# Optimization experiments

Hardware: AMD Instinct MI355X
Metric: run time of the kernel (lower is better)

The kernel has to match this reference:

```python
import jax, jax.numpy as jnp
import numpy as np

N, E, IN_DIM, HID, HEADS, LAYERS, NUM_STORES = 50000, 800000, 64, 128, 16, 3, 50
DH = HID // HEADS  # per-head dim = 8
EPS = 1e-5


def setup_inputs() -> dict:
    key = jax.random.key(0)
    ks = iter(jax.random.split(key, 40))
    def nrm(shape, scale):
        return jax.random.normal(next(ks), shape, dtype=jnp.float32) * scale
    inp = {}
    inp['x'] = jax.random.normal(next(ks), (N, IN_DIM), dtype=jnp.float32)
    inp['edge_index'] = jax.random.randint(next(ks), (2, E), 0, N, dtype=jnp.int32)
    inp['edge_weight'] = jax.random.uniform(next(ks), (E, 1), dtype=jnp.float32)
    inp['store_mask'] = jax.random.randint(next(ks), (N,), 0, NUM_STORES, dtype=jnp.int32)
    # input_proj: Linear + GELU + LayerNorm
    inp['in_W'] = nrm((IN_DIM, HID), IN_DIM ** -0.5)
    inp['in_b'] = jnp.zeros((HID,), jnp.float32)
    inp['in_g'] = jnp.ones((HID,), jnp.float32)
    inp['in_beta'] = jnp.zeros((HID,), jnp.float32)
    # 3 stacked GATv2 layers (stacked leading dim = layer)
    s = HID ** -0.5
    inp['gat_Wl'] = nrm((LAYERS, HID, HID), s)
    inp['gat_bl'] = jnp.zeros((LAYERS, HID), jnp.float32)
    inp['gat_Wr'] = nrm((LAYERS, HID, HID), s)
    inp['gat_br'] = jnp.zeros((LAYERS, HID), jnp.float32)
    inp['gat_We'] = nrm((LAYERS, 1, HID), 1.0)
    inp['gat_att'] = nrm((LAYERS, HEADS, DH), DH ** -0.5)
    inp['gat_bias'] = jnp.zeros((LAYERS, HID), jnp.float32)
    inp['blk_g'] = jnp.ones((LAYERS, HID), jnp.float32)
    inp['blk_b'] = jnp.zeros((LAYERS, HID), jnp.float32)
    # per-store context gate + final norm
    inp['ctx_W'] = nrm((HID, HID), s)
    inp['ctx_b'] = jnp.zeros((HID,), jnp.float32)
    inp['fin_g'] = jnp.ones((HID,), jnp.float32)
    inp['fin_b'] = jnp.zeros((HID,), jnp.float32)
    return inp


def layernorm(x, g, b):
    mu = jnp.mean(x, axis=-1, keepdims=True)
    v = jnp.mean((x - mu) ** 2, axis=-1, keepdims=True)
    return (x - mu) * jax.lax.rsqrt(v + EPS) * g + b


def gatv2_layer(x, src, dst, ea, Wl, bl, Wr, br, We, att, bias):
    # x: [N, HID]; src/dst: [Et]; ea: [Et, 1]
    n = x.shape[0]
    xl = (x @ Wl + bl).reshape(n, HEADS, DH)   # source transform
    xr = (x @ Wr + br).reshape(n, HEADS, DH)   # target transform
    ee = (ea @ We).reshape(-1, HEADS, DH)      # edge-attr embedding
    e = jax.nn.leaky_relu(xl[src] + xr[dst] + ee, 0.2)  # [Et, H, D]
    logit = jnp.einsum('ehd,hd->eh', e, att)             # [Et, H]
    # segment softmax over incoming edges of each target node
    mx = jax.ops.segment_max(logit, dst, num_segments=n)
    p = jnp.exp(logit - mx[dst])
    Z = jax.ops.segment_sum(p, dst, num_segments=n)
    alpha = p / (Z[dst] + 1e-16)
    msg = alpha[:, :, None] * xl[src]                    # [Et, H, D]
    agg = jax.ops.segment_sum(msg, dst, num_segments=n)  # [N, H, D]
    return agg.reshape(n, HEADS * DH) + bias


def forward(x, edge_index, edge_weight, store_mask, in_W, in_b, in_g, in_beta,
            gat_Wl, gat_bl, gat_Wr, gat_br, gat_We, gat_att, gat_bias,
            blk_g, blk_b, ctx_W, ctx_b, fin_g, fin_b):
    n = x.shape[0]
    h = layernorm(jax.nn.gelu(x @ in_W + in_b, approximate=False), in_g, in_beta)
    src, dst = edge_index[0], edge_index[1]
    # PyG add_self_loops with fill_value='mean': per-target mean of incoming edge attrs
    deg = jax.ops.segment_sum(jnp.ones(src.shape, h.dtype), dst, num_segments=n)
    loop_attr = jax.ops.segment_sum(edge_weight, dst, num_segments=n) / jnp.maximum(deg, 1.0)[:, None]
    loops = jnp.arange(n, dtype=src.dtype)
    srcf = jnp.concatenate([src, loops])
    dstf = jnp.concatenate([dst, loops])
    eaf = jnp.concatenate([edge_weight, loop_attr], axis=0)
    for l in range(LAYERS):  # residual block: post-norm residual around conv
        m = gatv2_layer(h, srcf, dstf, eaf, gat_Wl[l], gat_bl[l], gat_Wr[l], gat_br[l],
                        gat_We[l], gat_att[l], gat_bias[l])
        h = layernorm(h + m, blk_g[l], blk_b[l])
    # per-store segmented mean -> sigmoid gate -> scatter back
    cnt = jax.ops.segment_sum(jnp.ones((n,), h.dtype), store_mask, num_segments=NUM_STORES)
    means = jax.ops.segment_sum(h, store_mask, num_segments=NUM_STORES) / jnp.maximum(cnt, 1.0)[:, None]
    gate = jax.nn.sigmoid(means @ ctx_W + ctx_b)
    h = h + (gate * means)[store_mask]
    return layernorm(h, fin_g, fin_b)


def reference(x, edge_index, edge_weight, store_mask, in_W, in_b, in_g, in_beta,
              gat_Wl, gat_bl, gat_Wr, gat_br, gat_We, gat_att, gat_bias,
              blk_g, blk_b, ctx_W, ctx_b, fin_g, fin_b):
    return forward(x, edge_index, edge_weight, store_mask, in_W, in_b, in_g, in_beta,
                   gat_Wl, gat_bl, gat_Wr, gat_br, gat_We, gat_att, gat_bias,
                   blk_g, blk_b, ctx_W, ctx_b, fin_g, fin_b)
```

## Files before the change

### kernel.cpp

```cpp
#include <hip/hip_runtime.h>
#include <math.h>

#define NN 50000
#define EE 800000
#define ET (EE + NN)
#define HID 128
#define NSTORE 50
#define NBL 196
#define CNT_B 3125
#define WCV_B 192
#define IWC_B 32
#define SCT_B2 1661
#define GEMB 391
#define IPB 782
#define SSB 512
#define WB2 6250

typedef unsigned short ushort_t;
typedef unsigned int u32;
typedef __attribute__((ext_vector_type(8))) short bf8;
typedef __attribute__((ext_vector_type(4))) float f4;
typedef __attribute__((ext_vector_type(2))) float f2;
typedef __attribute__((ext_vector_type(4))) unsigned int u4;

__device__ __forceinline__ ushort_t f2b(float f) {
    union { float f; unsigned int i; } v; v.f = f;
    unsigned int r = (v.i + 0x7fffu + ((v.i >> 16) & 1u)) >> 16;
    return (ushort_t)r;
}
__device__ __forceinline__ f2 b2f2v(unsigned int u) {
    union { unsigned int i; float f; } lo, hi;
    lo.i = u << 16; hi.i = u & 0xffff0000u;
    f2 r; r.x = lo.f; r.y = hi.f; return r;
}
__device__ __forceinline__ unsigned int pk2(float lo, float hi) {
    return (unsigned int)f2b(lo) | ((unsigned int)f2b(hi) << 16);
}
__device__ __forceinline__ f2 max2(f2 a, f2 b) {
#if __has_builtin(__builtin_elementwise_max)
    return __builtin_elementwise_max(a, b);
#else
    f2 r; r.x = fmaxf(a.x, b.x); r.y = fmaxf(a.y, b.y); return r;
#endif
}

__global__ __launch_bounds__(256) void k_build(const int* __restrict__ ei, const float* __restrict__ ew,
                                               const float* __restrict__ inW,
                                               const float* __restrict__ gWl, const float* __restrict__ gWr,
                                               ushort_t* __restrict__ inWt,
                                               ushort_t* __restrict__ Wlt, ushort_t* __restrict__ Wrt,
                                               u32* __restrict__ packed, int* __restrict__ rank) {
    int b = blockIdx.x, t = threadIdx.x;
    if (b < CNT_B) {
        int i = b * 256 + t;
        int dst = ei[EE + i];
        unsigned int wfix = __float2uint_rn(ew[i] * 262144.0f);
        unsigned int old = atomicAdd(&packed[dst], (1u << 24) | wfix);
        rank[i] = (int)(old >> 24);
        return;
    }
    if (b < CNT_B + WCV_B) {
        int i = (b - CNT_B) * 256 + t;
        int l = i >> 14, r = i & 16383, nn2 = r >> 7, k = r & 127;
        Wlt[i] = f2b(gWl[(size_t)l * 16384 + k * 128 + nn2]);
        Wrt[i] = f2b(gWr[(size_t)l * 16384 + k * 128 + nn2]);
        return;
    }
    {
        int i = (b - CNT_B - WCV_B) * 256 + t;
        int c = i >> 6, k = i & 63;
        inWt[i] = f2b(inW[k * 128 + c]);
    }
}

__global__ __launch_bounds__(256) void k_psum(const u32* __restrict__ packed, int* __restrict__ bsum) {
    int t = threadIdx.x, bidx = blockIdx.x;
    int i = bidx * 256 + t;
    int v = (i < NN) ? (int)(packed[i] >> 24) + 1 : 0;
#pragma unroll
    for (int d = 1; d < 64; d <<= 1) v += __shfl_xor(v, d);
    __shared__ int ws4[4];
    if ((t & 63) == 0) ws4[t >> 6] = v;
    __syncthreads();
    if (t == 0) bsum[bidx] = ws4[0] + ws4[1] + ws4[2] + ws4[3];
}

__global__ __launch_bounds__(256) void k_offs2(const u32* __restrict__ packed,
                                               const int* __restrict__ bsum, int* __restrict__ offs) {
    __shared__ int bws[4];
    __shared__ int wsum4[4];
    int t = threadIdx.x, bidx = blockIdx.x;
    int i = bidx * 256 + t;
    int v = (i < NN) ? (int)(packed[i] >> 24) + 1 : 0;
    int lane = t & 63, w = t >> 6;

    int bv = (t < bidx) ? bsum[t] : 0;
#pragma unroll
    for (int d = 1; d < 64; d <<= 1) bv += __shfl_xor(bv, d);
    if (lane == 0) bws[w] = bv;

    int sc = v;
#pragma unroll
    for (int d = 1; d < 64; d <<= 1) {
        int u = __shfl_up(sc, d);
        if (lane >= d) sc += u;
    }
    if (lane == 63) wsum4[w] = sc;
    __syncthreads();
    int base = bws[0] + bws[1] + bws[2] + bws[3];
    int wo = 0;
    for (int k = 0; k < w; ++k) wo += wsum4[k];
    if (i < NN) offs[i] = base + wo + sc - v;
    if (bidx == 0 && t == 0) offs[NN] = ET;
}

__global__ __launch_bounds__(512) void k_inproj(const float* __restrict__ X,
                                                const ushort_t* __restrict__ Wt,
                                                const float* __restrict__ bias,
                                                const float* __restrict__ g,
                                                const float* __restrict__ be,
                                                ushort_t* __restrict__ hb) {
    const int K = 64;
    __shared__ float s1[2][64], s2[2][64];
    int t = threadIdx.x;
    int w = t >> 6, lane = t & 63;
    int cw = w & 1, rw = w >> 1;
    int q = lane >> 4, l16 = lane & 15;
    int row0 = blockIdx.x * 64 + rw * 16;
    int col0 = cw * 64;
    bf8 z; for (int k = 0; k < 8; ++k) z[k] = 0;

    bf8 bfr[2][4];
#pragma unroll
    for (int kk = 0; kk < 2; ++kk)
#pragma unroll
        for (int j = 0; j < 4; ++j)
            bfr[kk][j] = *(const bf8*)(Wt + (size_t)(col0 + j * 16 + l16) * K + kk * 32 + q * 8);

    f4 acc[4];
#pragma unroll
    for (int j = 0; j < 4; ++j) acc[j] = (f4)(0.f);

#pragma unroll
    for (int kk = 0; kk < 2; ++kk) {
        bf8 af;
        int r = row0 + l16;
        if (r < NN) {
            const float* xp = X + (size_t)r * K + kk * 32 + q * 8;
            f4 a = *(const f4*)xp;
            f4 c = *(const f4*)(xp + 4);
            u4 up; up.x = pk2(a.x, a.y); up.y = pk2(a.z, a.w);
            up.z = pk2(c.x, c.y); up.w = pk2(c.z, c.w);
            af = *(bf8*)&up;
        } else af = z;
#pragma unroll
        for (int j = 0; j < 4; ++j)
            acc[j] = __builtin_amdgcn_mfma_f32_16x16x32_bf16(af, bfr[kk][j], acc[j], 0, 0, 0);
    }
#pragma unroll
    for (int j = 0; j < 4; ++j) {
        float bv = bias[col0 + j * 16 + l16];
#pragma unroll
        for (int r = 0; r < 4; ++r) {
            float v = acc[j][r] + bv;
            v = 0.5f * v * (1.f + erff(v * 0.70710678118654752f));
            acc[j][r] = v;
        }
    }
#pragma unroll
    for (int r = 0; r < 4; ++r) {
        float sm = acc[0][r] + acc[1][r] + acc[2][r] + acc[3][r];
        float sq = acc[0][r] * acc[0][r] + acc[1][r] * acc[1][r]
                 + acc[2][r] * acc[2][r] + acc[3][r] * acc[3][r];
#pragma unroll
        for (int k = 1; k < 16; k <<= 1) { sm += __shfl_xor(sm, k); sq += __shfl_xor(sq, k); }
        if (l16 == 0) {
            int rl = rw * 16 + q * 4 + r;
            s1[cw][rl] = sm; s2[cw][rl] = sq;
        }
    }
    __syncthreads();
#pragma unroll
    for (int r = 0; r < 4; ++r) {
        int rl = rw * 16 + q * 4 + r;
        int gr = blockIdx.x * 64 + rl;
        if (gr >= NN) continue;
        float sm = s1[0][rl] + s1[1][rl];
        float sq = s2[0][rl] + s2[1][rl];
        float mu = sm * (1.f / 128.f);
        float var = sq * (1.f / 128.f) - mu * mu;
        float rinv = rsqrtf(var + 1e-5f);
#pragma unroll
        for (int j = 0; j < 4; ++j) {
            int gc = col0 + j * 16 + l16;
            float v = (acc[j][r] - mu) * rinv * g[gc] + be[gc];
            hb[(size_t)gr * HID + gc] = f2b(v);
        }
    }
}

__global__ __launch_bounds__(512) void k_gemm2(const ushort_t* __restrict__ A,
                                               const ushort_t* __restrict__ Wt0,
                                               const ushort_t* __restrict__ Wt1,
                                               const float* __restrict__ b0,
                                               const float* __restrict__ b1,
                                               ushort_t* __restrict__ o0,
                                               ushort_t* __restrict__ o1, int n,
                                               const int* __restrict__ ei,
                                               const float* __restrict__ ew,
                                               const int* __restrict__ offs,
                                               const u32* __restrict__ packed,
                                               const int* __restrict__ rank,
                                               int2* __restrict__ csr) {
    int bid = blockIdx.x;
    if (bid >= GEMB) {
        int i = (bid - GEMB) * 512 + threadIdx.x;
        if (i < EE) {
            int src = ei[i], dst = ei[EE + i];
            int pos = offs[dst] + rank[i];
            int2 v; v.x = src << 8; v.y = __float_as_int(ew[i]);
            csr[pos] = v;
        } else if (i < ET) {
            int nd = i - EE;
            u32 p = packed[nd];
            int deg = (int)(p >> 24);
            float wsf = (float)(p & 0xFFFFFFu) * (1.0f / 262144.0f);
            float la = wsf / fmaxf((float)deg, 1.0f);
            int pos = offs[nd + 1] - 1;
            int2 v; v.x = nd << 8; v.y = __float_as_int(la);
            csr[pos] = v;
        }
        return;
    }
    const int K = 128;
    __shared__ char As[128 * 256];
    int t = threadIdx.x;
    int row0 = bid * 128;
    bf8 z; for (int k = 0; k < 8; ++k) z[k] = 0;

    {
        int row = t >> 2, cq = t & 3;
        const ushort_t* srcp = A + (size_t)(row0 + row) * K + cq * 8;
        int swz = (row & 7) << 4;
        char* dst = As + row * 256;
        bool ok = (row0 + row) < n;
#pragma unroll
        for (int k = 0; k < 4; ++k) {
            bf8 v = ok ? *(const bf8*)(srcp + k * 32) : z;
            *(bf8*)(dst + ((k * 64 + cq * 16) ^ swz)) = v;
        }
    }
    __syncthreads();

    int w = t >> 6, lane = t & 63;
    int side = w >> 2, rw = (w >> 1) & 1, cw = w & 1;
    const ushort_t* Wt = side ? Wt1 : Wt0;
    const float* bias = side ? b1 : b0;
    ushort_t* outb = side ? o1 : o0;
    int q = lane >> 4, l16 = lane & 15;
    int col0 = cw * 64;

    f4 acc[4][4];
#pragma unroll
    for (int i = 0; i < 4; ++i)
#pragma unroll
        for (int j = 0; j < 4; ++j) acc[i][j] = (f4)(0.f);

#pragma unroll
    for (int kk = 0; kk < 4; ++kk) {
        bf8 bfk[4];
#pragma unroll
        for (int j = 0; j < 4; ++j)
            bfk[j] = *(const bf8*)(Wt + (size_t)(col0 + j * 16 + l16) * K + kk * 32 + q * 8);
        bf8 af[4];
#pragma unroll
        for (int i = 0; i < 4; ++i) {
            int r = rw * 64 + i * 16 + l16;
            af[i] = *(const bf8*)(As + r * 256 + ((kk * 64 + q * 16) ^ ((r & 7) << 4)));
        }
#pragma unroll
        for (int i = 0; i < 4; ++i)
#pragma unroll
            for (int j = 0; j < 4; ++j)
                acc[i][j] = __builtin_amdgcn_mfma_f32_16x16x32_bf16(af[i], bfk[j], acc[i][j], 0, 0, 0);
    }
#pragma unroll
    for (int i = 0; i < 4; ++i) {
        int gr0 = row0 + rw * 64 + i * 16 + q * 4;
#pragma unroll
        for (int j = 0; j < 4; ++j) {
            int gc = col0 + j * 16 + l16;
            float bv = bias[gc];
#pragma unroll
            for (int r = 0; r < 4; ++r) {
                int gr = gr0 + r;
                if (gr < n) outb[(size_t)gr * HID + gc] = f2b(acc[i][j][r] + bv);
            }
        }
    }
}

__global__ __launch_bounds__(256) void k_attn(const ushort_t* __restrict__ xl,
                                              const ushort_t* __restrict__ xr,
                                              ushort_t* __restrict__ hb,
                                              const int* __restrict__ offs,
                                              const int2* __restrict__ csr,
                                              const float* __restrict__ We,
                                              const float* __restrict__ att,
                                              const float* __restrict__ gbias,
                                              const float* __restrict__ g,
                                              const float* __restrict__ b,
                                              int n0) {
    int wid = n0 + ((blockIdx.x * 256 + threadIdx.x) >> 6);
    int lane = threadIdx.x & 63;
    if (wid >= NN) return;
    int hd = lane & 15;
    int grp = lane >> 4;
    int dbase = hd * 8;
    int db2 = hd * 16;
    size_t base = (size_t)wid * HID;

    f2 xr2[4], at2[4], we2[4];
    {
        u4 uxr = *(const u4*)(xr + base + dbase);
        xr2[0] = b2f2v(uxr.x); xr2[1] = b2f2v(uxr.y);
        xr2[2] = b2f2v(uxr.z); xr2[3] = b2f2v(uxr.w);
        f4 a0 = *(const f4*)(att + dbase), a1 = *(const f4*)(att + dbase + 4);
        at2[0].x = a0.x; at2[0].y = a0.y; at2[1].x = a0.z; at2[1].y = a0.w;
        at2[2].x = a1.x; at2[2].y = a1.y; at2[3].x = a1.z; at2[3].y = a1.w;
        f4 w0 = *(const f4*)(We + dbase), w1 = *(const f4*)(We + dbase + 4);
        we2[0].x = w0.x; we2[0].y = w0.y; we2[1].x = w0.z; we2[1].y = w0.w;
        we2[2].x = w1.x; we2[2].y = w1.y; we2[3].x = w1.z; we2[3].y = w1.w;
    }
    int p0 = offs[wid], p1 = offs[wid + 1];
    float Z = 0.f;
    f2 acc2[4];
#pragma unroll
    for (int q = 0; q < 4; ++q) { acc2[q].x = 0.f; acc2[q].y = 0.f; }

#define LOADQ(UX, EA, VM)                                                      \
    {                                                                          \
        int ei_ = e + grp;                                                     \
        VM = (ei_ < p1);                                                       \
        int2 m2_ = csr[VM ? ei_ : (p1 - 1)];                                   \
        EA = __int_as_float(m2_.y);                                            \
        UX = *(const u4*)((const char*)xl + (unsigned)m2_.x + db2);            \
    }

#define COMPQ(UX, EA, VM)                                                      \
    {                                                                          \
        f2 x2_[4];                                                             \
        x2_[0] = b2f2v(UX.x); x2_[1] = b2f2v(UX.y);                            \
        x2_[2] = b2f2v(UX.z); x2_[3] = b2f2v(UX.w);                            \
        f2 lg2_; lg2_.x = 0.f; lg2_.y = 0.f;                                   \
        _Pragma("unroll")                                                      \
        for (int q_ = 0; q_ < 4; ++q_) {                                       \
            f2 t_ = (x2_[q_] + xr2[q_]) + EA * we2[q_];                        \
            t_ = max2(t_, t_ * 0.2f);                                          \
            lg2_ += at2[q_] * t_;                                              \
        }                                                                      \
        float w_ = VM ? __expf(lg2_.x + lg2_.y) : 0.f;                         \
        Z += w_;                                                               \
        _Pragma("unroll")                                                      \
        for (int q_ = 0; q_ < 4; ++q_) acc2[q_] += w_ * x2_[q_];               \
    }

    {
        u4 uxA, uxB; float eaA, eaB; bool vA, vB;
        int e = p0;
        LOADQ(uxA, eaA, vA)
        e += 4;
        while (e < p1) {
            LOADQ(uxB, eaB, vB)
            e += 4;
            COMPQ(uxA, eaA, vA)
            if (e >= p1) { COMPQ(uxB, eaB, vB) goto redux; }
            LOADQ(uxA, eaA, vA)
            e += 4;
            COMPQ(uxB, eaB, vB)
        }
        COMPQ(uxA, eaA, vA)
    }
redux:;
#undef LOADQ
#undef COMPQ

    Z += __shfl_xor(Z, 16); Z += __shfl_xor(Z, 32);
#pragma unroll
    for (int q = 0; q < 4; ++q) {
        acc2[q].x += __shfl_xor(acc2[q].x, 16);
        acc2[q].x += __shfl_xor(acc2[q].x, 32);
        acc2[q].y += __shfl_xor(acc2[q].y, 16);
        acc2[q].y += __shfl_xor(acc2[q].y, 32);
    }
    float inv = 1.f / (Z + 1e-16f);
    float acc[8] = {acc2[0].x, acc2[0].y, acc2[1].x, acc2[1].y,
                    acc2[2].x, acc2[2].y, acc2[3].x, acc2[3].y};

    u4 uh = *(const u4*)(hb + base + dbase);
    f2 hr0 = b2f2v(uh.x), hr1 = b2f2v(uh.y), hr2 = b2f2v(uh.z), hr3 = b2f2v(uh.w);
    float hres[8] = {hr0.x, hr0.y, hr1.x, hr1.y, hr2.x, hr2.y, hr3.x, hr3.y};
    f4 gb0 = *(const f4*)(gbias + dbase), gb1 = *(const f4*)(gbias + dbase + 4);
    float gb8[8] = {gb0.x, gb0.y, gb0.z, gb0.w, gb1.x, gb1.y, gb1.z, gb1.w};
    float o[8], sm = 0.f, sq = 0.f;
#pragma unroll
    for (int q = 0; q < 8; ++q) {
        o[q] = acc[q] * inv + gb8[q] + hres[q];
        sm += o[q]; sq += o[q] * o[q];
    }
#pragma unroll
    for (int k = 1; k < 16; k <<= 1) { sm += __shfl_xor(sm, k); sq += __shfl_xor(sq, k); }
    float mu = sm * (1.f / 128.f);
    float var = sq * (1.f / 128.f) - mu * mu;
    float rinv = rsqrtf(var + 1e-5f);
    f4 g0 = *(const f4*)(g + dbase), g1 = *(const f4*)(g + dbase + 4);
    float g8[8] = {g0.x, g0.y, g0.z, g0.w, g1.x, g1.y, g1.z, g1.w};
    f4 b0 = *(const f4*)(b + dbase), b1 = *(const f4*)(b + dbase + 4);
    float b8[8] = {b0.x, b0.y, b0.z, b0.w, b1.x, b1.y, b1.z, b1.w};
    float v8[8];
#pragma unroll
    for (int q = 0; q < 8; ++q) v8[q] = (o[q] - mu) * rinv * g8[q] + b8[q];
    if (grp == 0) {
        u4 hu;
        hu.x = pk2(v8[0], v8[1]); hu.y = pk2(v8[2], v8[3]);
        hu.z = pk2(v8[4], v8[5]); hu.w = pk2(v8[6], v8[7]);
        *(u4*)(hb + base + dbase) = hu;
    }
}

__global__ __launch_bounds__(256) void k_store_sum(const ushort_t* __restrict__ hb,
                                                   const int* __restrict__ mask,
                                                   float* __restrict__ psums,
                                                   int* __restrict__ pcnts) {
    __shared__ float ls[NSTORE * HID];
    __shared__ int lc[NSTORE];
    int t = threadIdx.x, bidx = blockIdx.x;
    for (int i = t; i < NSTORE * HID; i += 256) ls[i] = 0.f;
    if (t < NSTORE) lc[t] = 0;
    __syncthreads();
    int wid = bidx * 4 + (t >> 6);
    int lane = t & 63;
    int nw = SSB * 4;
    int d0 = lane * 2;
    for (int node = wid; node < NN; node += nw) {
        int s = mask[node];
        unsigned int hv = ((const unsigned int*)(hb + (size_t)node * HID))[lane];
        f2 v = b2f2v(hv);
        atomicAdd(&ls[s * HID + d0], v.x);
        atomicAdd(&ls[s * HID + d0 + 1], v.y);
        if (lane == 0) atomicAdd(&lc[s], 1);
    }
    __syncthreads();
    for (int i = t; i < NSTORE * HID; i += 256) psums[(size_t)bidx * (NSTORE * HID) + i] = ls[i];
    if (t < NSTORE) pcnts[bidx * NSTORE + t] = lc[t];
}

__global__ __launch_bounds__(256) void k_gate(const float* __restrict__ psums,
                                              const int* __restrict__ pcnts,
                                              const float* __restrict__ ctxW,
                                              const float* __restrict__ ctxb,
                                              float* __restrict__ gm) {
    __shared__ float h1[HID];
    __shared__ float mloc[HID];
    __shared__ int cw4[4];
    int s = blockIdx.x, t = threadIdx.x;
    int d = t & 127, half = t >> 7;
    float s0 = 0.f, s1 = 0.f, s2 = 0.f, s3 = 0.f;
    for (int b = half * 4; b < SSB; b += 8) {
        s0 += psums[(size_t)(b + 0) * (NSTORE * HID) + s * HID + d];
        s1 += psums[(size_t)(b + 1) * (NSTORE * HID) + s * HID + d];
        s2 += psums[(size_t)(b + 2) * (NSTORE * HID) + s * HID + d];
        s3 += psums[(size_t)(b + 3) * (NSTORE * HID) + s * HID + d];
    }
    float sum = (s0 + s1) + (s2 + s3);
    int c = pcnts[t * NSTORE + s] + pcnts[(t + 256) * NSTORE + s];
#pragma unroll
    for (int k = 1; k < 64; k <<= 1) c += __shfl_xor(c, k);
    if ((t & 63) == 0) cw4[t >> 6] = c;
    if (half) h1[d] = sum;
    __syncthreads();
    if (half == 0) {
        float tot = sum + h1[d];
        float cnt = fmaxf((float)(cw4[0] + cw4[1] + cw4[2] + cw4[3]), 1.f);
        mloc[d] = tot / cnt;
    }
    __syncthreads();
    if (half == 0) {
        float acc = ctxb[d];
        for (int j = 0; j < HID; ++j) acc += mloc[j] * ctxW[j * HID + d];
        float gate = 1.f / (1.f + __expf(-acc));
        gm[s * HID + d] = gate * mloc[d];
    }
}

__global__ __launch_bounds__(256) void k_final(const ushort_t* __restrict__ hb,
                                               const int* __restrict__ mask,
                                               const float* __restrict__ gm,
                                               const float* __restrict__ g,
                                               const float* __restrict__ b,
                                               float* __restrict__ out) {
    int wid = (blockIdx.x * 256 + threadIdx.x) >> 6;
    int lane = threadIdx.x & 63;
    if (wid >= NN) return;
    size_t base = (size_t)wid * HID;
    int s = mask[wid];
    int d0 = lane * 2, d1 = d0 + 1;
    unsigned int hv = ((const unsigned int*)(hb + base))[lane];
    f2 hvv = b2f2v(hv);
    float v0 = hvv.x + gm[s * HID + d0];
    float v1 = hvv.y + gm[s * HID + d1];
    float sm = v0 + v1, sq = v0 * v0 + v1 * v1;
#pragma unroll
    for (int k = 1; k < 64; k <<= 1) { sm += __shfl_xor(sm, k); sq += __shfl_xor(sq, k); }
    float mu = sm * (1.f / 128.f);
    float var = sq * (1.f / 128.f) - mu * mu;
    float r = rsqrtf(var + 1e-5f);
    out[base + d0] = (v0 - mu) * r * g[d0] + b[d0];
    out[base + d1] = (v1 - mu) * r * g[d1] + b[d1];
}

extern "C" void kernel_launch(void* const* d_in, const int* in_sizes, int n_in,
                              void* d_out, int out_size, void* d_ws, size_t ws_size,
                              hipStream_t stream) {
    const float* x      = (const float*)d_in[0];
    const int*   ei     = (const int*)d_in[1];
    const float* ew     = (const float*)d_in[2];
    const int*   smask  = (const int*)d_in[3];
    const float* inW    = (const float*)d_in[4];
    const float* inb    = (const float*)d_in[5];
    const float* ing    = (const float*)d_in[6];
    const float* inbeta = (const float*)d_in[7];
    const float* gWl    = (const float*)d_in[8];
    const float* gbl    = (const float*)d_in[9];
    const float* gWr    = (const float*)d_in[10];
    const float* gbr    = (const float*)d_in[11];
    const float* gWe    = (const float*)d_in[12];
    const float* gatt   = (const float*)d_in[13];
    const float* gbias  = (const float*)d_in[14];
    const float* blkg   = (const float*)d_in[15];
    const float* blkb   = (const float*)d_in[16];
    const float* ctxW   = (const float*)d_in[17];
    const float* ctxb   = (const float*)d_in[18];
    const float* fing   = (const float*)d_in[19];
    const float* finb   = (const float*)d_in[20];
    float* out = (float*)d_out;

    float* ws = (float*)d_ws;
    size_t o = 0;
    int2*     csr    = (int2*)(ws + o);     o += (size_t)ET * 2;
    float*    gm     = ws + o;              o += NSTORE * HID;
    int*      offs   = (int*)(ws + o);      o += 50004;
    int*      rank   = (int*)(ws + o);      o += EE;
    ushort_t* hb     = (ushort_t*)(ws + o); o += (size_t)NN * HID / 2;
    ushort_t* xlb    = (ushort_t*)(ws + o); o += (size_t)NN * HID / 2;
    ushort_t* xrb    = (ushort_t*)(ws + o); o += (size_t)NN * HID / 2;
    ushort_t* inWt   = (ushort_t*)(ws + o); o += 128 * 64 / 2;
    ushort_t* Wlt    = (ushort_t*)(ws + o); o += 3 * 128 * 128 / 2;
    ushort_t* Wrt    = (ushort_t*)(ws + o); o += 3 * 128 * 128 / 2;
    int*      bsum   = (int*)(ws + o);      o += 256;
    float*    psums  = ws + o;              o += (size_t)SSB * NSTORE * HID;
    int*      pcnts  = (int*)(ws + o);      o += SSB * NSTORE;
    u32*      packed = (u32*)(ws + o);      o += NN;
    size_t zbytes = (size_t)NN * 4;

    hipMemsetAsync((void*)packed, 0, zbytes, stream);

    const int WB = NN / 4;

    k_build<<<CNT_B + WCV_B + IWC_B, 256, 0, stream>>>(ei, ew, inW, gWl, gWr,
                                                       inWt, Wlt, Wrt, packed, rank);
    k_psum<<<NBL, 256, 0, stream>>>(packed, bsum);
    k_offs2<<<NBL, 256, 0, stream>>>(packed, bsum, offs);
    k_inproj<<<IPB, 512, 0, stream>>>(x, inWt, inb, ing, inbeta, hb);

    for (int l = 0; l < 3; ++l) {
        int nb = GEMB + (l == 0 ? SCT_B2 : 0);
        k_gemm2<<<nb, 512, 0, stream>>>(hb, Wlt + (size_t)l * HID * HID, Wrt + (size_t)l * HID * HID,
                                        gbl + l * HID, gbr + l * HID, xlb, xrb, NN,
                                        ei, ew, offs, packed, rank, csr);
        k_attn<<<WB2, 256, 0, stream>>>(xlb, xrb, hb, offs, csr,
                                        gWe + l * HID, gatt + l * HID, gbias + l * HID,
                                        blkg + l * HID, blkb + l * HID, 0);
        k_attn<<<WB2, 256, 0, stream>>>(xlb, xrb, hb, offs, csr,
                                        gWe + l * HID, gatt + l * HID, gbias + l * HID,
                                        blkg + l * HID, blkb + l * HID, 25000);
    }

    k_store_sum<<<SSB, 256, 0, stream>>>(hb, smask, psums, pcnts);
    k_gate<<<NSTORE, 256, 0, stream>>>(psums, pcnts, ctxW, ctxb, gm);
    k_final<<<WB, 256, 0, stream>>>(hb, smask, gm, fing, finb, out);
}
```

Measured before the change: 476.9 us.

## Retile GEMM to 64-row blocks, merge attention launches, widen gate kernel

The dual-projection GEMM now uses 64-row tiles, with each wave computing 16 rows across all 128 columns instead of a 64x64 sub-tile. This doubles the block count for better occupancy and load balance. The two half-range attention launches per layer become a single launch. The store-gate reduction uses 1024 threads per block to shorten its serial psum loop, and the final LayerNorm writes float2 vectors. The trade-off is that each wave now reloads its weight fragments from global memory, and the smaller tiles reuse the A tile less.

```diff
diff --git a/kernel.cpp b/kernel.cpp
--- a/kernel.cpp
+++ b/kernel.cpp
@@ -11,10 +11,9 @@
 #define WCV_B 192
 #define IWC_B 32
 #define SCT_B2 1661
-#define GEMB 391
+#define GEMB2 782
 #define IPB 782
 #define SSB 512
-#define WB2 6250
 
 typedef unsigned short ushort_t;
 typedef unsigned int u32;
@@ -213,8 +212,8 @@
                                                const int* __restrict__ rank,
                                                int2* __restrict__ csr) {
     int bid = blockIdx.x;
-    if (bid >= GEMB) {
-        int i = (bid - GEMB) * 512 + threadIdx.x;
+    if (bid >= GEMB2) {
+        int i = (bid - GEMB2) * 512 + threadIdx.x;
         if (i < EE) {
             int src = ei[i], dst = ei[EE + i];
             int pos = offs[dst] + rank[i];
@@ -233,69 +232,58 @@
         return;
     }
     const int K = 128;
-    __shared__ char As[128 * 256];
+    __shared__ char As[64 * 256];
     int t = threadIdx.x;
-    int row0 = bid * 128;
+    int row0 = bid * 64;
     bf8 z; for (int k = 0; k < 8; ++k) z[k] = 0;
 
     {
-        int row = t >> 2, cq = t & 3;
-        const ushort_t* srcp = A + (size_t)(row0 + row) * K + cq * 8;
+        int row = t >> 3, cq = t & 7;
+        const ushort_t* srcp = A + (size_t)(row0 + row) * K + cq * 16;
         int swz = (row & 7) << 4;
         char* dst = As + row * 256;
         bool ok = (row0 + row) < n;
 #pragma unroll
-        for (int k = 0; k < 4; ++k) {
-            bf8 v = ok ? *(const bf8*)(srcp + k * 32) : z;
-            *(bf8*)(dst + ((k * 64 + cq * 16) ^ swz)) = v;
+        for (int k = 0; k < 2; ++k) {
+            bf8 v = ok ? *(const bf8*)(srcp + k * 8) : z;
+            *(bf8*)(dst + ((cq * 32 + k * 16) ^ swz)) = v;
         }
     }
     __syncthreads();
 
     int w = t >> 6, lane = t & 63;
-    int side = w >> 2, rw = (w >> 1) & 1, cw = w & 1;
+    int side = w >> 2, rw = w & 3;
     const ushort_t* Wt = side ? Wt1 : Wt0;
     const float* bias = side ? b1 : b0;
     ushort_t* outb = side ? o1 : o0;
     int q = lane >> 4, l16 = lane & 15;
-    int col0 = cw * 64;
-
-    f4 acc[4][4];
-#pragma unroll
-    for (int i = 0; i < 4; ++i)
-#pragma unroll
-        for (int j = 0; j < 4; ++j) acc[i][j] = (f4)(0.f);
+
+    f4 acc[8];
+#pragma unroll
+    for (int j = 0; j < 8; ++j) acc[j] = (f4)(0.f);
 
 #pragma unroll
     for (int kk = 0; kk < 4; ++kk) {
-        bf8 bfk[4];
-#pragma unroll
-        for (int j = 0; j < 4; ++j)
-            bfk[j] = *(const bf8*)(Wt + (size_t)(col0 + j * 16 + l16) * K + kk * 32 + q * 8);
-        bf8 af[4];
-#pragma unroll
-        for (int i = 0; i < 4; ++i) {
-            int r = rw * 64 + i * 16 + l16;
-            af[i] = *(const bf8*)(As + r * 256 + ((kk * 64 + q * 16) ^ ((r & 7) << 4)));
-        }
-#pragma unroll
-        for (int i = 0; i < 4; ++i)
-#pragma unroll
-            for (int j = 0; j < 4; ++j)
-                acc[i][j] = __builtin_amdgcn_mfma_f32_16x16x32_bf16(af[i], bfk[j], acc[i][j], 0, 0, 0);
-    }
-#pragma unroll
-    for (int i = 0; i < 4; ++i) {
-        int gr0 = row0 + rw * 64 + i * 16 + q * 4;
-#pragma unroll
-        for (int j = 0; j < 4; ++j) {
-            int gc = col0 + j * 16 + l16;
-            float bv = bias[gc];
-#pragma unroll
-            for (int r = 0; r < 4; ++r) {
-                int gr = gr0 + r;
-                if (gr < n) outb[(size_t)gr * HID + gc] = f2b(acc[i][j][r] + bv);
-            }
+        bf8 af;
+        {
+            int r = rw * 16 + l16;
+            af = *(const bf8*)(As + r * 256 + ((kk * 64 + q * 16) ^ ((r & 7) << 4)));
+        }
+#pragma unroll
+        for (int j = 0; j < 8; ++j) {
+            bf8 bfk = *(const bf8*)(Wt + (size_t)(j * 16 + l16) * K + kk * 32 + q * 8);
+            acc[j] = __builtin_amdgcn_mfma_f32_16x16x32_bf16(af, bfk, acc[j], 0, 0, 0);
+        }
+    }
+    int gr0 = row0 + rw * 16 + q * 4;
+#pragma unroll
+    for (int j = 0; j < 8; ++j) {
+        int gc = j * 16 + l16;
+        float bv = bias[gc];
+#pragma unroll
+        for (int r = 0; r < 4; ++r) {
+            int gr = gr0 + r;
+            if (gr < n) outb[(size_t)gr * HID + gc] = f2b(acc[j][r] + bv);
         }
     }
 }
@@ -309,9 +297,8 @@
                                               const float* __restrict__ att,
                                               const float* __restrict__ gbias,
                                               const float* __restrict__ g,
-                                              const float* __restrict__ b,
-                                              int n0) {
-    int wid = n0 + ((blockIdx.x * 256 + threadIdx.x) >> 6);
+                                              const float* __restrict__ b) {
+    int wid = (blockIdx.x * 256 + threadIdx.x) >> 6;
     int lane = threadIdx.x & 63;
     if (wid >= NN) return;
     int hd = lane & 15;
@@ -455,33 +442,39 @@
     if (t < NSTORE) pcnts[bidx * NSTORE + t] = lc[t];
 }
 
-__global__ __launch_bounds__(256) void k_gate(const float* __restrict__ psums,
-                                              const int* __restrict__ pcnts,
-                                              const float* __restrict__ ctxW,
-                                              const float* __restrict__ ctxb,
-                                              float* __restrict__ gm) {
-    __shared__ float h1[HID];
+__global__ __launch_bounds__(1024) void k_gate(const float* __restrict__ psums,
+                                               const int* __restrict__ pcnts,
+                                               const float* __restrict__ ctxW,
+                                               const float* __restrict__ ctxb,
+                                               float* __restrict__ gm) {
+    __shared__ float hpart[8][HID];
     __shared__ float mloc[HID];
-    __shared__ int cw4[4];
+    __shared__ int cw16[16];
     int s = blockIdx.x, t = threadIdx.x;
     int d = t & 127, half = t >> 7;
+    int lane = t & 63, wv = t >> 6;
     float s0 = 0.f, s1 = 0.f, s2 = 0.f, s3 = 0.f;
-    for (int b = half * 4; b < SSB; b += 8) {
+    for (int b = half * 4; b < SSB; b += 32) {
         s0 += psums[(size_t)(b + 0) * (NSTORE * HID) + s * HID + d];
         s1 += psums[(size_t)(b + 1) * (NSTORE * HID) + s * HID + d];
         s2 += psums[(size_t)(b + 2) * (NSTORE * HID) + s * HID + d];
         s3 += psums[(size_t)(b + 3) * (NSTORE * HID) + s * HID + d];
     }
     float sum = (s0 + s1) + (s2 + s3);
-    int c = pcnts[t * NSTORE + s] + pcnts[(t + 256) * NSTORE + s];
+    int c = (t < SSB) ? pcnts[t * NSTORE + s] : 0;
 #pragma unroll
     for (int k = 1; k < 64; k <<= 1) c += __shfl_xor(c, k);
-    if ((t & 63) == 0) cw4[t >> 6] = c;
-    if (half) h1[d] = sum;
+    if (lane == 0) cw16[wv] = c;
+    if (half) hpart[half][d] = sum;
     __syncthreads();
     if (half == 0) {
-        float tot = sum + h1[d];
-        float cnt = fmaxf((float)(cw4[0] + cw4[1] + cw4[2] + cw4[3]), 1.f);
+        float tot = sum;
+#pragma unroll
+        for (int h = 1; h < 8; ++h) tot += hpart[h][d];
+        int ct = 0;
+#pragma unroll
+        for (int k = 0; k < 16; ++k) ct += cw16[k];
+        float cnt = fmaxf((float)ct, 1.f);
         mloc[d] = tot / cnt;
     }
     __syncthreads();
@@ -515,8 +508,10 @@
     float mu = sm * (1.f / 128.f);
     float var = sq * (1.f / 128.f) - mu * mu;
     float r = rsqrtf(var + 1e-5f);
-    out[base + d0] = (v0 - mu) * r * g[d0] + b[d0];
-    out[base + d1] = (v1 - mu) * r * g[d1] + b[d1];
+    float2 ov;
+    ov.x = (v0 - mu) * r * g[d0] + b[d0];
+    ov.y = (v1 - mu) * r * g[d1] + b[d1];
+    *(float2*)(out + base + d0) = ov;
 }
 
 extern "C" void kernel_launch(void* const* d_in, const int* in_sizes, int n_in,
@@ -574,19 +569,16 @@
     k_inproj<<<IPB, 512, 0, stream>>>(x, inWt, inb, ing, inbeta, hb);
 
     for (int l = 0; l < 3; ++l) {
-        int nb = GEMB + (l == 0 ? SCT_B2 : 0);
+        int nb = GEMB2 + (l == 0 ? SCT_B2 : 0);
         k_gemm2<<<nb, 512, 0, stream>>>(hb, Wlt + (size_t)l * HID * HID, Wrt + (size_t)l * HID * HID,
                                         gbl + l * HID, gbr + l * HID, xlb, xrb, NN,
                                         ei, ew, offs, packed, rank, csr);
-        k_attn<<<WB2, 256, 0, stream>>>(xlb, xrb, hb, offs, csr,
-                                        gWe + l * HID, gatt + l * HID, gbias + l * HID,
-                                        blkg + l * HID, blkb + l * HID, 0);
-        k_attn<<<WB2, 256, 0, stream>>>(xlb, xrb, hb, offs, csr,
-                                        gWe + l * HID, gatt + l * HID, gbias + l * HID,
-                                        blkg + l * HID, blkb + l * HID, 25000);
+        k_attn<<<WB, 256, 0, stream>>>(xlb, xrb, hb, offs, csr,
+                                       gWe + l * HID, gatt + l * HID, gbias + l * HID,
+                                       blkg + l * HID, blkb + l * HID);
     }
 
     k_store_sum<<<SSB, 256, 0, stream>>>(hb, smask, psums, pcnts);
-    k_gate<<<NSTORE, 256, 0, stream>>>(psums, pcnts, ctxW, ctxb, gm);
+    k_gate<<<NSTORE, 1024, 0, stream>>>(psums, pcnts, ctxW, ctxb, gm);
     k_final<<<WB, 256, 0, stream>>>(hb, smask, gm, fing, finb, out);
 }
```

Measured after the change: 503.1 us. 5.5% more time.
